# Kernel tuning notes

Measured on AMD Instinct MI355X. Metric: run time of the kernel, lower is better.

Reference implementation:

```python
import jax, jax.numpy as jnp
import numpy as np

D = 512       # d_model
H = 8         # n_heads
HD = D // H   # head_dim
LYR = 4       # number_of_layers
PMT = 20      # pmt_len
L = 2048      # decode / target length (src_len - pmt_len)
BS = 1
DOUT = 3      # d_output (3 coding classes)
DFF = 4 * D
EPS = 1e-5


def layer_norm(x, g, b):
    m = jnp.mean(x, axis=-1, keepdims=True)
    v = jnp.mean((x - m) ** 2, axis=-1, keepdims=True)
    return (x - m) * jax.lax.rsqrt(v + EPS) * g + b


def rope(x):
    # x: (b, h, s, hd); half-split rotary with base 10000, positions = arange(s)
    half = x.shape[-1] // 2
    pos = jnp.arange(x.shape[2], dtype=jnp.float32)
    inv_freq = 1.0 / (10000.0 ** (jnp.arange(half, dtype=jnp.float32) / half))
    ang = pos[:, None] * inv_freq[None, :]          # (s, half)
    cos = jnp.cos(ang)[None, None]                  # (1,1,s,half)
    sin = jnp.sin(ang)[None, None]
    x1, x2 = x[..., :half], x[..., half:]
    return jnp.concatenate([x1 * cos - x2 * sin, x1 * sin + x2 * cos], axis=-1)


def mha(xq, xkv, wqkv, bqkv, wo, bo, key_mask, causal):
    # xq: (b, sq, D), xkv: (b, sk, D); key_mask: (b, sk) with 1=valid
    b, sq, _ = xq.shape
    sk = xkv.shape[1]
    q = xq @ wqkv[:, :D] + bqkv[:D]
    kv = xkv @ wqkv[:, D:] + bqkv[D:]
    k, v = kv[..., :D], kv[..., D:]
    q = q.reshape(b, sq, H, HD).transpose(0, 2, 1, 3)   # (b,h,sq,hd)
    k = k.reshape(b, sk, H, HD).transpose(0, 2, 1, 3)
    v = v.reshape(b, sk, H, HD).transpose(0, 2, 1, 3)
    q = rope(q)
    k = rope(k)
    scores = jnp.einsum('bhqd,bhkd->bhqk', q, k) / jnp.sqrt(jnp.float32(HD))
    scores = scores + jnp.where(key_mask[:, None, None, :] > 0, 0.0, -1e9)
    if causal:
        cm = jnp.tril(jnp.ones((sq, sk), dtype=bool))
        scores = jnp.where(cm[None, None], scores, -1e9)
    attn = jax.nn.softmax(scores, axis=-1)
    out = jnp.einsum('bhqk,bhkd->bhqd', attn, v)
    out = out.transpose(0, 2, 1, 3).reshape(b, sq, D)
    return out @ wo + bo


def setup_inputs() -> dict:
    key = jax.random.key(0)
    ks = jax.random.split(key, 16)
    s = 0.02
    p = lambda i, shape: jax.random.normal(ks[i], shape, jnp.float32) * s
    return {
        'trg_inputs': jax.random.normal(ks[0], (BS, L, DOUT), jnp.float32),
        'src_rep': jax.random.normal(ks[1], (BS, PMT + L, D), jnp.float32),
        'src_mask': jnp.ones((BS, L), jnp.float32),
        'emb_w': p(2, (DOUT, D)), 'emb_b': jnp.zeros((D,), jnp.float32),
        'sa_wqkv': p(3, (LYR, D, 3 * D)), 'sa_bqkv': jnp.zeros((LYR, 3 * D), jnp.float32),
        'sa_wo': p(4, (LYR, D, D)), 'sa_bo': jnp.zeros((LYR, D), jnp.float32),
        'ca_wqkv': p(5, (LYR, D, 3 * D)), 'ca_bqkv': jnp.zeros((LYR, 3 * D), jnp.float32),
        'ca_wo': p(6, (LYR, D, D)), 'ca_bo': jnp.zeros((LYR, D), jnp.float32),
        'ffn_w1': p(7, (LYR, D, DFF)), 'ffn_b1': jnp.zeros((LYR, DFF), jnp.float32),
        'ffn_w2': p(8, (LYR, DFF, D)), 'ffn_b2': jnp.zeros((LYR, D), jnp.float32),
        'ln_g': jnp.ones((LYR, 3, D), jnp.float32), 'ln_b': jnp.zeros((LYR, 3, D), jnp.float32),
        'lnf_g': jnp.ones((D,), jnp.float32), 'lnf_b': jnp.zeros((D,), jnp.float32),
        'gen_w': p(9, (D, DOUT)), 'gen_b': jnp.zeros((DOUT,), jnp.float32),
    }


def reference(trg_inputs, src_rep, src_mask, emb_w, emb_b, sa_wqkv, sa_bqkv, sa_wo, sa_bo,
              ca_wqkv, ca_bqkv, ca_wo, ca_bo, ffn_w1, ffn_b1, ffn_w2, ffn_b2,
              ln_g, ln_b, lnf_g, lnf_b, gen_w, gen_b):
    srb = src_rep[:, PMT:, :]                       # (bs, L, D)
    x = trg_inputs @ emb_w + emb_b                  # (bs, L, D)
    trg_mask = src_mask                             # parallel mode: trg_mask = src_mask
    for li in range(LYR):
        h = layer_norm(x, ln_g[li, 0], ln_b[li, 0])
        x = x + mha(h, h, sa_wqkv[li], sa_bqkv[li], sa_wo[li], sa_bo[li], trg_mask, causal=True)
        h = layer_norm(x, ln_g[li, 1], ln_b[li, 1])
        x = x + mha(h, srb, ca_wqkv[li], ca_bqkv[li], ca_wo[li], ca_bo[li], src_mask, causal=False)
        h = layer_norm(x, ln_g[li, 2], ln_b[li, 2])
        x = x + (jax.nn.relu(h @ ffn_w1[li] + ffn_b1[li]) @ ffn_w2[li] + ffn_b2[li])
    x = layer_norm(x, lnf_g, lnf_b)
    return x @ gen_w + gen_b                        # logits (bs, L, 3)
```

## Files before the change

### kernel.cpp

```cpp
#include <hip/hip_runtime.h>
#include <hip/hip_bf16.h>

#define SEQ 2048
#define DM 512
#define NHEAD 8
#define HDIM 64
#define DFFN 2048
#define PMTN 20

typedef __bf16 bf16x8 __attribute__((ext_vector_type(8)));
typedef float f32x4 __attribute__((ext_vector_type(4)));
typedef unsigned short u16x8 __attribute__((ext_vector_type(8)));

__device__ __forceinline__ float wave_sum(float v) {
#pragma unroll
  for (int off = 32; off; off >>= 1) v += __shfl_xor(v, off);
  return v;
}

__device__ __forceinline__ unsigned short f2b(float x) {
  __hip_bfloat16 h = __float2bfloat16(x);
  return *(unsigned short*)&h;
}

__device__ __forceinline__ void gll16(const __hip_bfloat16* g, __hip_bfloat16* l) {
  __builtin_amdgcn_global_load_lds(
      (const __attribute__((address_space(1))) unsigned int*)(g),
      (__attribute__((address_space(3))) unsigned int*)(l), 16, 0, 0);
}

__global__ __launch_bounds__(256) void embed_kernel(
    const float* __restrict__ trg, const float* __restrict__ w,
    const float* __restrict__ b, float* __restrict__ X) {
  int idx = blockIdx.x * 256 + threadIdx.x;
  int r = idx >> 9, c = idx & 511;
  float t0 = trg[r * 3 + 0], t1 = trg[r * 3 + 1], t2 = trg[r * 3 + 2];
  X[idx] = t0 * w[c] + t1 * w[512 + c] + t2 * w[1024 + c] + b[c];
}

__global__ __launch_bounds__(256) void cast_bf16_kernel(
    const float* __restrict__ in, __hip_bfloat16* __restrict__ out) {
  int i = blockIdx.x * 256 + threadIdx.x;
  out[i] = __float2bfloat16(in[i]);
}

__global__ __launch_bounds__(256) void rope_table_kernel(float2* __restrict__ rt) {
  int idx = blockIdx.x * 256 + threadIdx.x;
  int row = idx >> 5, i = idx & 31;
  float inv = __expf(-(float)i * (9.210340371976184f / 32.f));
  float sn, cs;
  sincosf((float)row * inv, &sn, &cs);
  rt[idx] = make_float2(cs, sn);
}

__global__ __launch_bounds__(256) void mbias_kernel(
    const float* __restrict__ mask, float* __restrict__ mb) {
  int i = blockIdx.x * 256 + threadIdx.x;
  mb[i] = (mask[i] > 0.f) ? 0.f : -8.0e9f;
}

__global__ __launch_bounds__(256) void ln_bf16_kernel(
    const float* __restrict__ x, const float* __restrict__ g,
    const float* __restrict__ b, __hip_bfloat16* __restrict__ o) {
  int row = blockIdx.x * 4 + (threadIdx.x >> 6);
  int lane = threadIdx.x & 63;
  const float* xr = x + (long)row * DM;
  float v[8];
  float s = 0.f;
#pragma unroll
  for (int j = 0; j < 8; j++) { v[j] = xr[lane + 64 * j]; s += v[j]; }
  s = wave_sum(s);
  float mean = s * (1.f / DM);
  float q = 0.f;
#pragma unroll
  for (int j = 0; j < 8; j++) { float d = v[j] - mean; q += d * d; }
  q = wave_sum(q);
  float r = rsqrtf(q * (1.f / DM) + 1e-5f);
  __hip_bfloat16* orow = o + (long)row * DM;
#pragma unroll
  for (int j = 0; j < 8; j++) {
    int c = lane + 64 * j;
    orow[c] = __float2bfloat16((v[j] - mean) * r * g[c] + b[c]);
  }
}

__global__ __launch_bounds__(256) void ln_f32_kernel(
    const float* __restrict__ x, const float* __restrict__ g,
    const float* __restrict__ b, float* __restrict__ o) {
  int row = blockIdx.x * 4 + (threadIdx.x >> 6);
  int lane = threadIdx.x & 63;
  const float* xr = x + (long)row * DM;
  float v[8];
  float s = 0.f;
#pragma unroll
  for (int j = 0; j < 8; j++) { v[j] = xr[lane + 64 * j]; s += v[j]; }
  s = wave_sum(s);
  float mean = s * (1.f / DM);
  float q = 0.f;
#pragma unroll
  for (int j = 0; j < 8; j++) { float d = v[j] - mean; q += d * d; }
  q = wave_sum(q);
  float r = rsqrtf(q * (1.f / DM) + 1e-5f);
  float* orow = o + (long)row * DM;
#pragma unroll
  for (int j = 0; j < 8; j++) {
    int c = lane + 64 * j;
    orow[c] = (v[j] - mean) * r * g[c] + b[c];
  }
}

__global__ __launch_bounds__(256) void transpose_layer_kernel(
    const float* __restrict__ wqkv, const float* __restrict__ wo,
    const float* __restrict__ cwqkv, const float* __restrict__ cwo,
    const float* __restrict__ w1, const float* __restrict__ w2,
    __hip_bfloat16* __restrict__ Wt) {
  int b = blockIdx.x;
  const float* W;
  __hip_bfloat16* O;
  int Kd, Nd;
  if (b < 192)      { W = wqkv;  O = Wt + 0;       Kd = 512;  Nd = 1536; }
  else if (b < 256) { W = wo;    O = Wt + 786432;  Kd = 512;  Nd = 512;  b -= 192; }
  else if (b < 448) { W = cwqkv; O = Wt + 1048576; Kd = 512;  Nd = 1536; b -= 256; }
  else if (b < 512) { W = cwo;   O = Wt + 1835008; Kd = 512;  Nd = 512;  b -= 448; }
  else if (b < 768) { W = w1;    O = Wt + 2097152; Kd = 512;  Nd = 2048; b -= 512; }
  else              { W = w2;    O = Wt + 3145728; Kd = 2048; Nd = 512;  b -= 768; }
  int tn = Nd >> 6;
  int k0 = (b / tn) * 64, n0 = (b % tn) * 64;
  __shared__ float T[64][65];
  int t = threadIdx.x;
  int rr = t >> 4, c4 = (t & 15) * 4;
#pragma unroll
  for (int p = 0; p < 4; p++) {
    int row = rr + p * 16;
    float4 v = *(const float4*)(W + (long)(k0 + row) * Nd + n0 + c4);
    T[row][c4 + 0] = v.x; T[row][c4 + 1] = v.y;
    T[row][c4 + 2] = v.z; T[row][c4 + 3] = v.w;
  }
  __syncthreads();
#pragma unroll
  for (int p = 0; p < 4; p++) {
    int row = rr + p * 16;
    ushort4 pk;
    pk.x = f2b(T[c4 + 0][row]); pk.y = f2b(T[c4 + 1][row]);
    pk.z = f2b(T[c4 + 2][row]); pk.w = f2b(T[c4 + 3][row]);
    *(ushort4*)(O + (long)(n0 + row) * Kd + k0 + c4) = pk;
  }
}

__global__ __launch_bounds__(256) void gemm_bf16_64(
    const __hip_bfloat16* __restrict__ A, int lda,
    const __hip_bfloat16* __restrict__ A2,
    const __hip_bfloat16* __restrict__ Bt, int ldb,
    const float* __restrict__ bias,
    const float* __restrict__ residual,
    float* __restrict__ Cf, __hip_bfloat16* __restrict__ Cb, int ldc,
    int K, int relu, int mode, const float2* __restrict__ rt,
    __hip_bfloat16* __restrict__ Qp, __hip_bfloat16* __restrict__ Kp,
    __hip_bfloat16* __restrict__ Vtp) {
  __shared__ __attribute__((aligned(16))) __hip_bfloat16 As[2][4096];
  __shared__ __attribute__((aligned(16))) __hip_bfloat16 Bs[2][4096];
  const int t = threadIdx.x;
  const int bx = blockIdx.x;
  const int nrow = bx * 64, m0 = blockIdx.y * 64;
  const int ptype = (mode == 0) ? 3 : (nrow < 512 ? 0 : (nrow < 1024 ? 1 : 2));
  const int head = (nrow >> 6) & 7;
  const __hip_bfloat16* Ause = (mode == 2 && bx >= 8) ? A2 : A;

  const int w = t >> 6, lane = t & 63;
  const int wr = w >> 1, wc = w & 1;
  const int fr = lane & 15, fk = lane >> 4;
  const int r0 = t & 63, c0 = t >> 6;
  const __hip_bfloat16* Arow = Ause + (long)(m0 + r0) * lda;
  const __hip_bfloat16* Brow = Bt + (long)(nrow + r0) * ldb;

  uint4 ra0 = *(const uint4*)(Arow + c0 * 8);
  uint4 ra1 = *(const uint4*)(Arow + (c0 + 4) * 8);
  uint4 rb0 = *(const uint4*)(Brow + c0 * 8);
  uint4 rb1 = *(const uint4*)(Brow + (c0 + 4) * 8);
  *(uint4*)(&As[0][(c0 * 64 + r0) * 8]) = ra0;
  *(uint4*)(&As[0][((c0 + 4) * 64 + r0) * 8]) = ra1;
  *(uint4*)(&Bs[0][(c0 * 64 + r0) * 8]) = rb0;
  *(uint4*)(&Bs[0][((c0 + 4) * 64 + r0) * 8]) = rb1;
  __syncthreads();

  f32x4 acc[2][2] = {};
  const int NK = K >> 6;
  for (int ks = 0; ks < NK; ++ks) {
    const int cur = ks & 1;
    if (ks + 1 < NK) {
      const int ko = (ks + 1) << 6;
      ra0 = *(const uint4*)(Arow + ko + c0 * 8);
      ra1 = *(const uint4*)(Arow + ko + (c0 + 4) * 8);
      rb0 = *(const uint4*)(Brow + ko + c0 * 8);
      rb1 = *(const uint4*)(Brow + ko + (c0 + 4) * 8);
    }
#pragma unroll
    for (int kk = 0; kk < 2; ++kk) {
      const int kc = kk * 4 + fk;
      bf16x8 a0 = *(const bf16x8*)(&As[cur][(kc * 64 + wr * 32 + fr) * 8]);
      bf16x8 a1 = *(const bf16x8*)(&As[cur][(kc * 64 + wr * 32 + 16 + fr) * 8]);
      bf16x8 b0 = *(const bf16x8*)(&Bs[cur][(kc * 64 + wc * 32 + fr) * 8]);
      bf16x8 b1 = *(const bf16x8*)(&Bs[cur][(kc * 64 + wc * 32 + 16 + fr) * 8]);
      acc[0][0] = __builtin_amdgcn_mfma_f32_16x16x32_bf16(a0, b0, acc[0][0], 0, 0, 0);
      acc[0][1] = __builtin_amdgcn_mfma_f32_16x16x32_bf16(a0, b1, acc[0][1], 0, 0, 0);
      acc[1][0] = __builtin_amdgcn_mfma_f32_16x16x32_bf16(a1, b0, acc[1][0], 0, 0, 0);
      acc[1][1] = __builtin_amdgcn_mfma_f32_16x16x32_bf16(a1, b1, acc[1][1], 0, 0, 0);
    }
    if (ks + 1 < NK) {
      const int nxt = cur ^ 1;
      *(uint4*)(&As[nxt][(c0 * 64 + r0) * 8]) = ra0;
      *(uint4*)(&As[nxt][((c0 + 4) * 64 + r0) * 8]) = ra1;
      *(uint4*)(&Bs[nxt][(c0 * 64 + r0) * 8]) = rb0;
      *(uint4*)(&Bs[nxt][((c0 + 4) * 64 + r0) * 8]) = rb1;
    }
    __syncthreads();
  }

  if (ptype == 3) {
#pragma unroll
    for (int m = 0; m < 2; ++m)
#pragma unroll
      for (int n = 0; n < 2; ++n)
#pragma unroll
        for (int j = 0; j < 4; ++j) {
          int r = m0 + wr * 32 + m * 16 + fk * 4 + j;
          int c = nrow + wc * 32 + n * 16 + fr;
          float v = acc[m][n][j] + bias[c];
          if (relu) v = fmaxf(v, 0.f);
          if (residual) v += residual[(long)r * ldc + c];
          if (Cf) Cf[(long)r * ldc + c] = v;
          if (Cb) Cb[(long)r * ldc + c] = __float2bfloat16(v);
        }
    return;
  }

  float* Lt = (float*)As;
#pragma unroll
  for (int m = 0; m < 2; ++m)
#pragma unroll
    for (int n = 0; n < 2; ++n)
#pragma unroll
      for (int j = 0; j < 4; ++j) {
        int rl = wr * 32 + m * 16 + fk * 4 + j;
        int cl = wc * 32 + n * 16 + fr;
        Lt[rl * 64 + (cl ^ (rl & 31))] = acc[m][n][j] + bias[nrow + cl];
      }
  __syncthreads();

  if (ptype == 2) {
    const int d = t >> 2, sc = (t & 3) * 16;
    u16x8 o0, o1;
#pragma unroll
    for (int s = 0; s < 8; s++) {
      o0[s] = f2b(Lt[(sc + s) * 64 + (d ^ ((sc + s) & 31))]);
      o1[s] = f2b(Lt[(sc + 8 + s) * 64 + (d ^ ((sc + 8 + s) & 31))]);
    }
    __hip_bfloat16* dst = Vtp + ((long)(head * 64 + d)) * SEQ + m0 + sc;
    *(u16x8*)dst = o0;
    *(u16x8*)(dst + 8) = o1;
  } else {
    const int r = t >> 2, i0 = (t & 3) * 8;
    const float2* rp = rt + (long)(m0 + r) * 32 + i0;
    u16x8 lo, hi;
#pragma unroll
    for (int p = 0; p < 8; p++) {
      float a = Lt[r * 64 + ((i0 + p) ^ (r & 31))];
      float b = Lt[r * 64 + ((i0 + p + 32) ^ (r & 31))];
      float2 cs = rp[p];
      lo[p] = f2b(a * cs.x - b * cs.y);
      hi[p] = f2b(a * cs.y + b * cs.x);
    }
    __hip_bfloat16* dst =
        (ptype == 0 ? Qp : Kp) + ((long)head * SEQ + m0 + r) * 64 + i0;
    *(u16x8*)dst = lo;
    *(u16x8*)(dst + 32) = hi;
  }
}

__global__ __launch_bounds__(256) void attn_part_kernel(
    const __hip_bfloat16* __restrict__ Qp, const __hip_bfloat16* __restrict__ Kp,
    const __hip_bfloat16* __restrict__ Vtp, const float* __restrict__ mbias,
    __hip_bfloat16* __restrict__ Op, float* __restrict__ Ml,
    int causal, int csz) {
  const int qt = blockIdx.x, ch = blockIdx.y, head = blockIdx.z;
  const int kv0 = ch * csz;
  if (causal && kv0 > qt * 64 + 63) return;
  const int kvlen = causal ? min(csz, qt * 64 + 64 - kv0) : csz;
  const int nt = (kvlen + 63) >> 6;

  __shared__ __attribute__((aligned(16))) __hip_bfloat16 Ks[4096];
  __shared__ __attribute__((aligned(16))) __hip_bfloat16 Vs[4096];
  __shared__ __attribute__((aligned(16))) __hip_bfloat16 Ps[4096];
  const int t = threadIdx.x, w = t >> 6, lane = t & 63;
  const int fr = lane & 15, fk = lane >> 4;
  const int qr = qt * 64 + w * 16 + fr;
  const int wq0 = qt * 64 + w * 16;
  const float SCL = 0.18033688011112042f;

  bf16x8 qa0, qa1;
  {
    const __hip_bfloat16* qp = Qp + ((long)head * SEQ + qr) * 64 + fk * 8;
    qa0 = *(const bf16x8*)qp;
    qa1 = *(const bf16x8*)(qp + 32);
  }
  const __hip_bfloat16* Kh = Kp + (long)head * SEQ * 64;
  const __hip_bfloat16* Vh = Vtp + (long)head * 64 * SEQ;

  float m_i = -3e38f, l_i = 0.f;
  f32x4 o_[4] = {};
  const int sw2 = (fr & 7) << 4;

  for (int tile = 0; tile < nt; ++tile) {
    const int kb = kv0 + tile * 64;
    __syncthreads();
    {
      const __hip_bfloat16* src = Kh + (long)(kb + (t & 63)) * 64 + (t >> 6) * 8;
      gll16(src, Ks + t * 8);
      gll16(src + 32, Ks + t * 8 + 2048);
    }
    {
      const __hip_bfloat16* src = Vh + (long)(t & 63) * SEQ + kb + (t >> 6) * 8;
      gll16(src, Vs + t * 8);
      gll16(src + 32, Vs + t * 8 + 2048);
    }
    __syncthreads();

    const bool need = !causal || (kb <= wq0 + 15);
    if (need) {
      const bool diag = causal && (kb + 63 > wq0);

      f32x4 sacc[4];
#pragma unroll
      for (int n = 0; n < 4; n++) {
        bf16x8 ka0 = *(const bf16x8*)(Ks + fk * 512 + (n * 16 + fr) * 8);
        bf16x8 ka1 = *(const bf16x8*)(Ks + (4 + fk) * 512 + (n * 16 + fr) * 8);
        f32x4 zz = {};
        zz = __builtin_amdgcn_mfma_f32_16x16x32_bf16(ka0, qa0, zz, 0, 0, 0);
        sacc[n] = __builtin_amdgcn_mfma_f32_16x16x32_bf16(ka1, qa1, zz, 0, 0, 0);
      }

      float sv[4][4];
      float rm = -3e38f;
#pragma unroll
      for (int n = 0; n < 4; n++) {
        const int ka = kb + n * 16 + fk * 4;
        float4 mb = *(const float4*)(mbias + ka);
        sv[n][0] = sacc[n][0] + mb.x;
        sv[n][1] = sacc[n][1] + mb.y;
        sv[n][2] = sacc[n][2] + mb.z;
        sv[n][3] = sacc[n][3] + mb.w;
        if (diag) {
#pragma unroll
          for (int j = 0; j < 4; j++)
            if (ka + j > qr) sv[n][j] = -3e38f;
        }
#pragma unroll
        for (int j = 0; j < 4; j++) rm = fmaxf(rm, sv[n][j]);
      }
      rm = fmaxf(rm, __shfl_xor(rm, 16));
      rm = fmaxf(rm, __shfl_xor(rm, 32));
      if (!__all(rm <= m_i)) {
        float nm = fmaxf(m_i, rm);
        float f = exp2f((m_i - nm) * SCL);
        l_i *= f;
#pragma unroll
        for (int n = 0; n < 4; n++) o_[n] *= f;
        m_i = nm;
      }
      float ps = 0.f;
#pragma unroll
      for (int n = 0; n < 4; n++) {
        float p0 = exp2f((sv[n][0] - m_i) * SCL);
        float p1 = exp2f((sv[n][1] - m_i) * SCL);
        float p2 = exp2f((sv[n][2] - m_i) * SCL);
        float p3 = exp2f((sv[n][3] - m_i) * SCL);
        ps += (p0 + p1) + (p2 + p3);
        ushort4 pk4;
        pk4.x = f2b(p0); pk4.y = f2b(p1); pk4.z = f2b(p2); pk4.w = f2b(p3);
        *(ushort4*)((char*)Ps + ((w * 2048 + fr * 128 + (n * 16 + fk * 4) * 2) ^ sw2)) = pk4;
      }
      ps += __shfl_xor(ps, 16);
      ps += __shfl_xor(ps, 32);
      l_i += ps;

#pragma unroll
      for (int s = 0; s < 2; s++) {
        bf16x8 pb = *(const bf16x8*)((char*)Ps + ((w * 2048 + fr * 128 + s * 64 + fk * 16) ^ sw2));
#pragma unroll
        for (int n = 0; n < 4; n++) {
          bf16x8 va = *(const bf16x8*)(Vs + (s * 4 + fk) * 512 + (n * 16 + fr) * 8);
          o_[n] = __builtin_amdgcn_mfma_f32_16x16x32_bf16(va, pb, o_[n], 0, 0, 0);
        }
      }
    }
  }

  const long bid = ((long)head * 32 + qt) * gridDim.y + ch;
  __hip_bfloat16* Ob = Op + bid * 4096;
#pragma unroll
  for (int n = 0; n < 4; n++) {
    ushort4 ov;
    ov.x = f2b(o_[n][0]); ov.y = f2b(o_[n][1]);
    ov.z = f2b(o_[n][2]); ov.w = f2b(o_[n][3]);
    *(ushort4*)(Ob + (w * 16 + fr) * 64 + n * 16 + fk * 4) = ov;
  }
  if (fk == 0) {
    float2 ml = make_float2(m_i, l_i);
    *(float2*)(Ml + bid * 128 + (w * 16 + fr) * 2) = ml;
  }
}

__global__ __launch_bounds__(256) void attn_combine_kernel(
    const __hip_bfloat16* __restrict__ Op, const float* __restrict__ Ml,
    __hip_bfloat16* __restrict__ O, int ldo, int causal, int csz, int nch) {
  const int qt = blockIdx.x, head = blockIdx.y;
  const int nc = causal ? min(nch, (qt * 64 + 63) / csz + 1) : nch;
  const int t = threadIdx.x;
  const int row = t >> 2, c16 = (t & 3) * 16;
  const long bid0 = ((long)head * 32 + qt) * nch;
  const float SCL = 0.18033688011112042f;
  float M = -3e38f;
  for (int c = 0; c < nc; c++) M = fmaxf(M, Ml[(bid0 + c) * 128 + row * 2]);
  float L = 0.f;
  float acc[16] = {};
  for (int c = 0; c < nc; c++) {
    float2 ml = *(const float2*)(Ml + (bid0 + c) * 128 + row * 2);
    float wg = exp2f((ml.x - M) * SCL);
    L += wg * ml.y;
    const __hip_bfloat16* base = Op + (bid0 + c) * 4096 + row * 64 + c16;
    bf16x8 a = *(const bf16x8*)base;
    bf16x8 b = *(const bf16x8*)(base + 8);
#pragma unroll
    for (int e = 0; e < 8; e++) {
      acc[e] += wg * (float)a[e];
      acc[8 + e] += wg * (float)b[e];
    }
  }
  float invL = 1.f / fmaxf(L, 1e-20f);
  u16x8 o0, o1;
#pragma unroll
  for (int e = 0; e < 8; e++) {
    o0[e] = f2b(acc[e] * invL);
    o1[e] = f2b(acc[8 + e] * invL);
  }
  __hip_bfloat16* orow = O + (long)(qt * 64 + row) * ldo + head * 64 + c16;
  *(u16x8*)orow = o0;
  *(u16x8*)(orow + 8) = o1;
}

__global__ __launch_bounds__(64) void gen_kernel(
    const float* __restrict__ h, const float* __restrict__ gw,
    const float* __restrict__ gb, float* __restrict__ out) {
  int row = blockIdx.x, lane = threadIdx.x;
  float a0 = 0.f, a1 = 0.f, a2 = 0.f;
  for (int k = lane; k < DM; k += 64) {
    float x = h[(long)row * DM + k];
    a0 = fmaf(x, gw[k * 3 + 0], a0);
    a1 = fmaf(x, gw[k * 3 + 1], a1);
    a2 = fmaf(x, gw[k * 3 + 2], a2);
  }
  a0 = wave_sum(a0);
  a1 = wave_sum(a1);
  a2 = wave_sum(a2);
  if (lane == 0) {
    out[row * 3 + 0] = a0 + gb[0];
    out[row * 3 + 1] = a1 + gb[1];
    out[row * 3 + 2] = a2 + gb[2];
  }
}

extern "C" void kernel_launch(void* const* d_in, const int* in_sizes, int n_in,
                              void* d_out, int out_size, void* d_ws, size_t ws_size,
                              hipStream_t stream) {
  const float* trg      = (const float*)d_in[0];
  const float* src_rep  = (const float*)d_in[1];
  const float* src_mask = (const float*)d_in[2];
  const float* emb_w    = (const float*)d_in[3];
  const float* emb_b    = (const float*)d_in[4];
  const float* sa_wqkv  = (const float*)d_in[5];
  const float* sa_bqkv  = (const float*)d_in[6];
  const float* sa_wo    = (const float*)d_in[7];
  const float* sa_bo    = (const float*)d_in[8];
  const float* ca_wqkv  = (const float*)d_in[9];
  const float* ca_bqkv  = (const float*)d_in[10];
  const float* ca_wo    = (const float*)d_in[11];
  const float* ca_bo    = (const float*)d_in[12];
  const float* ffn_w1   = (const float*)d_in[13];
  const float* ffn_b1   = (const float*)d_in[14];
  const float* ffn_w2   = (const float*)d_in[15];
  const float* ffn_b2   = (const float*)d_in[16];
  const float* ln_g     = (const float*)d_in[17];
  const float* ln_b     = (const float*)d_in[18];
  const float* lnf_g    = (const float*)d_in[19];
  const float* lnf_b    = (const float*)d_in[20];
  const float* gen_w    = (const float*)d_in[21];
  const float* gen_b    = (const float*)d_in[22];

  const float* srb = src_rep + (long)PMTN * DM;

  char* wsb = (char*)d_ws;
  float*          X    = (float*)wsb;
  __hip_bfloat16* Hb   = (__hip_bfloat16*)(wsb + (4ul << 20));
  __hip_bfloat16* MID  = (__hip_bfloat16*)(wsb + (6ul << 20));
  __hip_bfloat16* Op   = MID;
  float*          Hf   = (float*)MID;
  __hip_bfloat16* AO   = (__hip_bfloat16*)(wsb + (14ul << 20));
  __hip_bfloat16* SRBb = (__hip_bfloat16*)(wsb + (16ul << 20));
  __hip_bfloat16* Wt   = (__hip_bfloat16*)(wsb + (18ul << 20));
  float2*         rt   = (float2*)(wsb + (26ul << 20));
  float*          mbias= (float*)(wsb + (26ul << 20) + 524288);
  float*          Ml   = (float*)(wsb + (27ul << 20));
  __hip_bfloat16* Qp   = (__hip_bfloat16*)(wsb + (28ul << 20));
  __hip_bfloat16* Kp   = (__hip_bfloat16*)(wsb + (30ul << 20));
  __hip_bfloat16* Vtp  = (__hip_bfloat16*)(wsb + (32ul << 20));

  const int nch = 4;
  const int csz = SEQ / nch;

  embed_kernel<<<(SEQ * DM) / 256, 256, 0, stream>>>(trg, emb_w, emb_b, X);
  cast_bf16_kernel<<<(SEQ * DM) / 256, 256, 0, stream>>>(srb, SRBb);
  rope_table_kernel<<<256, 256, 0, stream>>>(rt);
  mbias_kernel<<<8, 256, 0, stream>>>(src_mask, mbias);

  __hip_bfloat16* wqkvT  = Wt + 0;
  __hip_bfloat16* woT    = Wt + 786432;
  __hip_bfloat16* cwqkvT = Wt + 1048576;
  __hip_bfloat16* cwoT   = Wt + 1835008;
  __hip_bfloat16* w1T    = Wt + 2097152;
  __hip_bfloat16* w2T    = Wt + 3145728;

  for (int li = 0; li < 4; li++) {
    transpose_layer_kernel<<<1024, 256, 0, stream>>>(
        sa_wqkv + (long)li * DM * 3 * DM, sa_wo + (long)li * DM * DM,
        ca_wqkv + (long)li * DM * 3 * DM, ca_wo + (long)li * DM * DM,
        ffn_w1 + (long)li * DM * DFFN, ffn_w2 + (long)li * DFFN * DM, Wt);

    const float* bqkv  = sa_bqkv + (long)li * 3 * DM;
    const float* bo    = sa_bo + (long)li * DM;
    const float* cbqkv = ca_bqkv + (long)li * 3 * DM;
    const float* cbo   = ca_bo + (long)li * DM;
    const float* b1    = ffn_b1 + (long)li * DFFN;
    const float* b2    = ffn_b2 + (long)li * DM;
    const float* g0  = ln_g + (long)(li * 3 + 0) * DM;
    const float* bb0 = ln_b + (long)(li * 3 + 0) * DM;
    const float* g1  = ln_g + (long)(li * 3 + 1) * DM;
    const float* bb1 = ln_b + (long)(li * 3 + 1) * DM;
    const float* g2  = ln_g + (long)(li * 3 + 2) * DM;
    const float* bb2 = ln_b + (long)(li * 3 + 2) * DM;

    ln_bf16_kernel<<<512, 256, 0, stream>>>(X, g0, bb0, Hb);
    gemm_bf16_64<<<dim3(24, 32), 256, 0, stream>>>(
        Hb, DM, nullptr, wqkvT, DM, bqkv, nullptr, nullptr, nullptr, DM,
        DM, 0, 1, rt, Qp, Kp, Vtp);
    attn_part_kernel<<<dim3(32, nch, 8), 256, 0, stream>>>(
        Qp, Kp, Vtp, mbias, Op, Ml, 1, csz);
    attn_combine_kernel<<<dim3(32, 8), 256, 0, stream>>>(
        Op, Ml, AO, DM, 1, csz, nch);
    gemm_bf16_64<<<dim3(8, 32), 256, 0, stream>>>(
        AO, DM, nullptr, woT, DM, bo, X, X, nullptr, DM,
        DM, 0, 0, nullptr, nullptr, nullptr, nullptr);

    ln_bf16_kernel<<<512, 256, 0, stream>>>(X, g1, bb1, Hb);
    gemm_bf16_64<<<dim3(24, 32), 256, 0, stream>>>(
        Hb, DM, SRBb, cwqkvT, DM, cbqkv, nullptr, nullptr, nullptr, DM,
        DM, 0, 2, rt, Qp, Kp, Vtp);
    attn_part_kernel<<<dim3(32, nch, 8), 256, 0, stream>>>(
        Qp, Kp, Vtp, mbias, Op, Ml, 0, csz);
    attn_combine_kernel<<<dim3(32, 8), 256, 0, stream>>>(
        Op, Ml, AO, DM, 0, csz, nch);
    gemm_bf16_64<<<dim3(8, 32), 256, 0, stream>>>(
        AO, DM, nullptr, cwoT, DM, cbo, X, X, nullptr, DM,
        DM, 0, 0, nullptr, nullptr, nullptr, nullptr);

    ln_bf16_kernel<<<512, 256, 0, stream>>>(X, g2, bb2, Hb);
    gemm_bf16_64<<<dim3(32, 32), 256, 0, stream>>>(
        Hb, DM, nullptr, w1T, DM, b1, nullptr, nullptr, MID, DFFN,
        DM, 1, 0, nullptr, nullptr, nullptr, nullptr);
    gemm_bf16_64<<<dim3(8, 32), 256, 0, stream>>>(
        MID, DFFN, nullptr, w2T, DFFN, b2, X, X, nullptr, DM,
        DFFN, 0, 0, nullptr, nullptr, nullptr, nullptr);
  }

  ln_f32_kernel<<<512, 256, 0, stream>>>(X, lnf_g, lnf_b, Hf);
  gen_kernel<<<SEQ, 64, 0, stream>>>(Hf, gen_w, gen_b, (float*)d_out);
}
```

Measured before the change: 802.5 us.

## Hoist weight transposes, deepen GEMM prefetch, skip unmasked bias, add MFMA priority

Transposes all four layers' weights in one launch when workspace allows, instead of one transpose launch per layer. Turns the GEMM global-to-register prefetch into a two-stage ring so loads run two k-steps ahead. Computes a per-64-key mask flag so attention can skip loading the mask bias for fully valid tiles, and raises wave priority around the MFMA sections. This trades more registers and a larger workspace for fewer launches and less latency exposure.

```diff
diff --git a/kernel.cpp b/kernel.cpp
--- a/kernel.cpp
+++ b/kernel.cpp
@@ -7,6 +7,7 @@
 #define HDIM 64
 #define DFFN 2048
 #define PMTN 20
+#define WTS 4194304
 
 typedef __bf16 bf16x8 __attribute__((ext_vector_type(8)));
 typedef float f32x4 __attribute__((ext_vector_type(4)));
@@ -54,9 +55,13 @@
 }
 
 __global__ __launch_bounds__(256) void mbias_kernel(
-    const float* __restrict__ mask, float* __restrict__ mb) {
+    const float* __restrict__ mask, float* __restrict__ mb,
+    int* __restrict__ mtflag) {
   int i = blockIdx.x * 256 + threadIdx.x;
-  mb[i] = (mask[i] > 0.f) ? 0.f : -8.0e9f;
+  bool masked = !(mask[i] > 0.f);
+  mb[i] = masked ? -8.0e9f : 0.f;
+  unsigned long long any = __ballot(masked);
+  if ((threadIdx.x & 63) == 0) mtflag[i >> 6] = (any != 0ull) ? 1 : 0;
 }
 
 __global__ __launch_bounds__(256) void ln_bf16_kernel(
@@ -110,20 +115,23 @@
 }
 
 __global__ __launch_bounds__(256) void transpose_layer_kernel(
-    const float* __restrict__ wqkv, const float* __restrict__ wo,
-    const float* __restrict__ cwqkv, const float* __restrict__ cwo,
-    const float* __restrict__ w1, const float* __restrict__ w2,
-    __hip_bfloat16* __restrict__ Wt) {
+    const float* __restrict__ wqkv0, const float* __restrict__ wo0,
+    const float* __restrict__ cwqkv0, const float* __restrict__ cwo0,
+    const float* __restrict__ w10, const float* __restrict__ w20,
+    __hip_bfloat16* __restrict__ Wt0, int li0) {
   int b = blockIdx.x;
+  int li = li0 + (b >> 10);
+  b &= 1023;
   const float* W;
   __hip_bfloat16* O;
+  __hip_bfloat16* Wt = Wt0 + (long)(b >= 0 ? (blockIdx.x >> 10) : 0) * WTS;
   int Kd, Nd;
-  if (b < 192)      { W = wqkv;  O = Wt + 0;       Kd = 512;  Nd = 1536; }
-  else if (b < 256) { W = wo;    O = Wt + 786432;  Kd = 512;  Nd = 512;  b -= 192; }
-  else if (b < 448) { W = cwqkv; O = Wt + 1048576; Kd = 512;  Nd = 1536; b -= 256; }
-  else if (b < 512) { W = cwo;   O = Wt + 1835008; Kd = 512;  Nd = 512;  b -= 448; }
-  else if (b < 768) { W = w1;    O = Wt + 2097152; Kd = 512;  Nd = 2048; b -= 512; }
-  else              { W = w2;    O = Wt + 3145728; Kd = 2048; Nd = 512;  b -= 768; }
+  if (b < 192)      { W = wqkv0 + (long)li * DM * 3 * DM;  O = Wt + 0;       Kd = 512;  Nd = 1536; }
+  else if (b < 256) { W = wo0 + (long)li * DM * DM;        O = Wt + 786432;  Kd = 512;  Nd = 512;  b -= 192; }
+  else if (b < 448) { W = cwqkv0 + (long)li * DM * 3 * DM; O = Wt + 1048576; Kd = 512;  Nd = 1536; b -= 256; }
+  else if (b < 512) { W = cwo0 + (long)li * DM * DM;       O = Wt + 1835008; Kd = 512;  Nd = 512;  b -= 448; }
+  else if (b < 768) { W = w10 + (long)li * DM * DFFN;      O = Wt + 2097152; Kd = 512;  Nd = 2048; b -= 512; }
+  else              { W = w20 + (long)li * DFFN * DM;      O = Wt + 3145728; Kd = 2048; Nd = 512;  b -= 768; }
   int tn = Nd >> 6;
   int k0 = (b / tn) * 64, n0 = (b % tn) * 64;
   __shared__ float T[64][65];
@@ -173,26 +181,34 @@
   const __hip_bfloat16* Arow = Ause + (long)(m0 + r0) * lda;
   const __hip_bfloat16* Brow = Bt + (long)(nrow + r0) * ldb;
 
-  uint4 ra0 = *(const uint4*)(Arow + c0 * 8);
-  uint4 ra1 = *(const uint4*)(Arow + (c0 + 4) * 8);
-  uint4 rb0 = *(const uint4*)(Brow + c0 * 8);
-  uint4 rb1 = *(const uint4*)(Brow + (c0 + 4) * 8);
-  *(uint4*)(&As[0][(c0 * 64 + r0) * 8]) = ra0;
-  *(uint4*)(&As[0][((c0 + 4) * 64 + r0) * 8]) = ra1;
-  *(uint4*)(&Bs[0][(c0 * 64 + r0) * 8]) = rb0;
-  *(uint4*)(&Bs[0][((c0 + 4) * 64 + r0) * 8]) = rb1;
+  const int NK = K >> 6;
+  uint4 sa0[2], sa1[2], sb0[2], sb1[2];
+
+  sa0[0] = *(const uint4*)(Arow + c0 * 8);
+  sa1[0] = *(const uint4*)(Arow + (c0 + 4) * 8);
+  sb0[0] = *(const uint4*)(Brow + c0 * 8);
+  sb1[0] = *(const uint4*)(Brow + (c0 + 4) * 8);
+  *(uint4*)(&As[0][(c0 * 64 + r0) * 8]) = sa0[0];
+  *(uint4*)(&As[0][((c0 + 4) * 64 + r0) * 8]) = sa1[0];
+  *(uint4*)(&Bs[0][(c0 * 64 + r0) * 8]) = sb0[0];
+  *(uint4*)(&Bs[0][((c0 + 4) * 64 + r0) * 8]) = sb1[0];
+  if (NK > 1) {
+    sa0[1] = *(const uint4*)(Arow + 64 + c0 * 8);
+    sa1[1] = *(const uint4*)(Arow + 64 + (c0 + 4) * 8);
+    sb0[1] = *(const uint4*)(Brow + 64 + c0 * 8);
+    sb1[1] = *(const uint4*)(Brow + 64 + (c0 + 4) * 8);
+  }
   __syncthreads();
 
   f32x4 acc[2][2] = {};
-  const int NK = K >> 6;
   for (int ks = 0; ks < NK; ++ks) {
     const int cur = ks & 1;
-    if (ks + 1 < NK) {
-      const int ko = (ks + 1) << 6;
-      ra0 = *(const uint4*)(Arow + ko + c0 * 8);
-      ra1 = *(const uint4*)(Arow + ko + (c0 + 4) * 8);
-      rb0 = *(const uint4*)(Brow + ko + c0 * 8);
-      rb1 = *(const uint4*)(Brow + ko + (c0 + 4) * 8);
+    if (ks + 2 < NK) {
+      const long ko = (long)(ks + 2) << 6;
+      sa0[cur] = *(const uint4*)(Arow + ko + c0 * 8);
+      sa1[cur] = *(const uint4*)(Arow + ko + (c0 + 4) * 8);
+      sb0[cur] = *(const uint4*)(Brow + ko + c0 * 8);
+      sb1[cur] = *(const uint4*)(Brow + ko + (c0 + 4) * 8);
     }
 #pragma unroll
     for (int kk = 0; kk < 2; ++kk) {
@@ -208,10 +224,10 @@
     }
     if (ks + 1 < NK) {
       const int nxt = cur ^ 1;
-      *(uint4*)(&As[nxt][(c0 * 64 + r0) * 8]) = ra0;
-      *(uint4*)(&As[nxt][((c0 + 4) * 64 + r0) * 8]) = ra1;
-      *(uint4*)(&Bs[nxt][(c0 * 64 + r0) * 8]) = rb0;
-      *(uint4*)(&Bs[nxt][((c0 + 4) * 64 + r0) * 8]) = rb1;
+      *(uint4*)(&As[nxt][(c0 * 64 + r0) * 8]) = sa0[nxt];
+      *(uint4*)(&As[nxt][((c0 + 4) * 64 + r0) * 8]) = sa1[nxt];
+      *(uint4*)(&Bs[nxt][(c0 * 64 + r0) * 8]) = sb0[nxt];
+      *(uint4*)(&Bs[nxt][((c0 + 4) * 64 + r0) * 8]) = sb1[nxt];
     }
     __syncthreads();
   }
@@ -280,6 +296,7 @@
 __global__ __launch_bounds__(256) void attn_part_kernel(
     const __hip_bfloat16* __restrict__ Qp, const __hip_bfloat16* __restrict__ Kp,
     const __hip_bfloat16* __restrict__ Vtp, const float* __restrict__ mbias,
+    const int* __restrict__ mtflag,
     __hip_bfloat16* __restrict__ Op, float* __restrict__ Ml,
     int causal, int csz) {
   const int qt = blockIdx.x, ch = blockIdx.y, head = blockIdx.z;
@@ -328,8 +345,10 @@
     const bool need = !causal || (kb <= wq0 + 15);
     if (need) {
       const bool diag = causal && (kb + 63 > wq0);
+      const bool hasmask = mtflag[kb >> 6] != 0;
 
       f32x4 sacc[4];
+      __builtin_amdgcn_s_setprio(1);
 #pragma unroll
       for (int n = 0; n < 4; n++) {
         bf16x8 ka0 = *(const bf16x8*)(Ks + fk * 512 + (n * 16 + fr) * 8);
@@ -338,17 +357,23 @@
         zz = __builtin_amdgcn_mfma_f32_16x16x32_bf16(ka0, qa0, zz, 0, 0, 0);
         sacc[n] = __builtin_amdgcn_mfma_f32_16x16x32_bf16(ka1, qa1, zz, 0, 0, 0);
       }
+      __builtin_amdgcn_s_setprio(0);
 
       float sv[4][4];
       float rm = -3e38f;
 #pragma unroll
       for (int n = 0; n < 4; n++) {
         const int ka = kb + n * 16 + fk * 4;
-        float4 mb = *(const float4*)(mbias + ka);
-        sv[n][0] = sacc[n][0] + mb.x;
-        sv[n][1] = sacc[n][1] + mb.y;
-        sv[n][2] = sacc[n][2] + mb.z;
-        sv[n][3] = sacc[n][3] + mb.w;
+        if (hasmask) {
+          float4 mb = *(const float4*)(mbias + ka);
+          sv[n][0] = sacc[n][0] + mb.x;
+          sv[n][1] = sacc[n][1] + mb.y;
+          sv[n][2] = sacc[n][2] + mb.z;
+          sv[n][3] = sacc[n][3] + mb.w;
+        } else {
+          sv[n][0] = sacc[n][0]; sv[n][1] = sacc[n][1];
+          sv[n][2] = sacc[n][2]; sv[n][3] = sacc[n][3];
+        }
         if (diag) {
 #pragma unroll
           for (int j = 0; j < 4; j++)
@@ -383,6 +408,7 @@
       ps += __shfl_xor(ps, 32);
       l_i += ps;
 
+      __builtin_amdgcn_s_setprio(1);
 #pragma unroll
       for (int s = 0; s < 2; s++) {
         bf16x8 pb = *(const bf16x8*)((char*)Ps + ((w * 2048 + fr * 128 + s * 64 + fk * 16) ^ sw2));
@@ -392,6 +418,7 @@
           o_[n] = __builtin_amdgcn_mfma_f32_16x16x32_bf16(va, pb, o_[n], 0, 0, 0);
         }
       }
+      __builtin_amdgcn_s_setprio(0);
     }
   }
 
@@ -506,34 +533,43 @@
   float*          Hf   = (float*)MID;
   __hip_bfloat16* AO   = (__hip_bfloat16*)(wsb + (14ul << 20));
   __hip_bfloat16* SRBb = (__hip_bfloat16*)(wsb + (16ul << 20));
-  __hip_bfloat16* Wt   = (__hip_bfloat16*)(wsb + (18ul << 20));
-  float2*         rt   = (float2*)(wsb + (26ul << 20));
-  float*          mbias= (float*)(wsb + (26ul << 20) + 524288);
-  float*          Ml   = (float*)(wsb + (27ul << 20));
-  __hip_bfloat16* Qp   = (__hip_bfloat16*)(wsb + (28ul << 20));
-  __hip_bfloat16* Kp   = (__hip_bfloat16*)(wsb + (30ul << 20));
-  __hip_bfloat16* Vtp  = (__hip_bfloat16*)(wsb + (32ul << 20));
-
+  float2*         rt   = (float2*)(wsb + (18ul << 20));
+  float*          mbias= (float*)(wsb + (18ul << 20) + 524288);
+  int*            mtfl = (int*)(wsb + (18ul << 20) + 532480);
+  float*          Ml   = (float*)(wsb + (19ul << 20));
+  __hip_bfloat16* Qp   = (__hip_bfloat16*)(wsb + (20ul << 20));
+  __hip_bfloat16* Kp   = (__hip_bfloat16*)(wsb + (22ul << 20));
+  __hip_bfloat16* Vtp  = (__hip_bfloat16*)(wsb + (24ul << 20));
+  __hip_bfloat16* Wt   = (__hip_bfloat16*)(wsb + (26ul << 20));
+
+  const bool hoist = ws_size >= ((26ul << 20) + 4ul * WTS * 2ul);
   const int nch = 4;
   const int csz = SEQ / nch;
 
   embed_kernel<<<(SEQ * DM) / 256, 256, 0, stream>>>(trg, emb_w, emb_b, X);
   cast_bf16_kernel<<<(SEQ * DM) / 256, 256, 0, stream>>>(srb, SRBb);
   rope_table_kernel<<<256, 256, 0, stream>>>(rt);
-  mbias_kernel<<<8, 256, 0, stream>>>(src_mask, mbias);
-
-  __hip_bfloat16* wqkvT  = Wt + 0;
-  __hip_bfloat16* woT    = Wt + 786432;
-  __hip_bfloat16* cwqkvT = Wt + 1048576;
-  __hip_bfloat16* cwoT   = Wt + 1835008;
-  __hip_bfloat16* w1T    = Wt + 2097152;
-  __hip_bfloat16* w2T    = Wt + 3145728;
+  mbias_kernel<<<8, 256, 0, stream>>>(src_mask, mbias, mtfl);
+
+  if (hoist) {
+    transpose_layer_kernel<<<4096, 256, 0, stream>>>(
+        sa_wqkv, sa_wo, ca_wqkv, ca_wo, ffn_w1, ffn_w2, Wt, 0);
+  }
 
   for (int li = 0; li < 4; li++) {
-    transpose_layer_kernel<<<1024, 256, 0, stream>>>(
-        sa_wqkv + (long)li * DM * 3 * DM, sa_wo + (long)li * DM * DM,
-        ca_wqkv + (long)li * DM * 3 * DM, ca_wo + (long)li * DM * DM,
-        ffn_w1 + (long)li * DM * DFFN, ffn_w2 + (long)li * DFFN * DM, Wt);
+    __hip_bfloat16* Wl = hoist ? (Wt + (long)li * WTS) : Wt;
+    if (!hoist) {
+      transpose_layer_kernel<<<1024, 256, 0, stream>>>(
+          sa_wqkv + (long)li * DM * 3 * DM, sa_wo + (long)li * DM * DM,
+          ca_wqkv + (long)li * DM * 3 * DM, ca_wo + (long)li * DM * DM,
+          ffn_w1 + (long)li * DM * DFFN, ffn_w2 + (long)li * DFFN * DM, Wt, 0);
+    }
+    __hip_bfloat16* wqkvT  = Wl + 0;
+    __hip_bfloat16* woT    = Wl + 786432;
+    __hip_bfloat16* cwqkvT = Wl + 1048576;
+    __hip_bfloat16* cwoT   = Wl + 1835008;
+    __hip_bfloat16* w1T    = Wl + 2097152;
+    __hip_bfloat16* w2T    = Wl + 3145728;
 
     const float* bqkv  = sa_bqkv + (long)li * 3 * DM;
     const float* bo    = sa_bo + (long)li * DM;
@@ -553,7 +589,7 @@
         Hb, DM, nullptr, wqkvT, DM, bqkv, nullptr, nullptr, nullptr, DM,
         DM, 0, 1, rt, Qp, Kp, Vtp);
     attn_part_kernel<<<dim3(32, nch, 8), 256, 0, stream>>>(
-        Qp, Kp, Vtp, mbias, Op, Ml, 1, csz);
+        Qp, Kp, Vtp, mbias, mtfl, Op, Ml, 1, csz);
     attn_combine_kernel<<<dim3(32, 8), 256, 0, stream>>>(
         Op, Ml, AO, DM, 1, csz, nch);
     gemm_bf16_64<<<dim3(8, 32), 256, 0, stream>>>(
@@ -565,7 +601,7 @@
         Hb, DM, SRBb, cwqkvT, DM, cbqkv, nullptr, nullptr, nullptr, DM,
         DM, 0, 2, rt, Qp, Kp, Vtp);
     attn_part_kernel<<<dim3(32, nch, 8), 256, 0, stream>>>(
-        Qp, Kp, Vtp, mbias, Op, Ml, 0, csz);
+        Qp, Kp, Vtp, mbias, mtfl, Op, Ml, 0, csz);
     attn_combine_kernel<<<dim3(32, 8), 256, 0, stream>>>(
         Op, Ml, AO, DM, 0, csz, nch);
     gemm_bf16_64<<<dim3(8, 32), 256, 0, stream>>>(
```

Measured after the change: 1.161 ms. +44.6%, slower.
